# Optimization experiments

Hardware: AMD Instinct MI355X
Metric: run time of the kernel (lower is better)

The kernel has to match this reference:

```python
import jax, jax.numpy as jnp
import numpy as np

ALPHA = 0.2  # LeakyReLU negative slope
NEG_INF = -1e9


def setup_inputs() -> dict:
    key = jax.random.key(0)
    k1, k2, k3, k4 = jax.random.split(key, 4)
    B, N, IN, OUT = 8, 2048, 512, 32
    graph_input = jax.random.normal(k1, (B, N, IN), dtype=jnp.float32)
    adj = jax.random.randint(k2, (B, N, N), 0, 2, dtype=jnp.int32)
    W_fc = jax.random.normal(k3, (OUT, IN), dtype=jnp.float32) * (1.0 / np.sqrt(IN))
    W_attn = jax.random.normal(k4, (1, 2 * OUT), dtype=jnp.float32) * (1.0 / np.sqrt(2 * OUT))
    return {"graph_input": graph_input, "adj": adj, "W_fc": W_fc, "W_attn": W_attn}


def reference(graph_input, adj, W_fc, W_attn):
    # h: [B, N, 32]
    h = jnp.einsum('bni,oi->bno', graph_input, W_fc)
    out_dim = W_fc.shape[0]
    # attn_fc(cat(h_i, h_j)) is separable: a1.h_i + a2.h_j
    a1 = W_attn[0, :out_dim]   # [32]
    a2 = W_attn[0, out_dim:]   # [32]
    f1 = jnp.einsum('bno,o->bn', h, a1)  # [B, N]
    f2 = jnp.einsum('bno,o->bn', h, a2)  # [B, N]
    scores = jax.nn.leaky_relu(f1[:, :, None] + f2[:, None, :], negative_slope=ALPHA)  # [B,N,N]
    scores = jnp.where(adj == 0, NEG_INF, scores)
    attn = jax.nn.softmax(scores, axis=2)
    # NOTE: original multiplies attention with graph_input (not h)
    h_prime = jnp.einsum('bnm,bmi->bni', attn, graph_input)  # [B, N, IN]
    return jax.nn.elu(h_prime)  # concat=True path
```

## Files before the change

### kernel.cpp

```cpp
#include <hip/hip_runtime.h>
#include <hip/hip_bf16.h>

#define BATCH 8
#define NN    2048
#define FIN   512
#define FOUT  32
#define GALPHA 0.2f
#define NROW  128
#define NIT   32

typedef float  f32x4  __attribute__((ext_vector_type(4)));
typedef __bf16 bf16x8 __attribute__((ext_vector_type(8)));
typedef unsigned short u16;
typedef u16 u16x8 __attribute__((ext_vector_type(8)));

static __device__ __forceinline__ u16 f2bf(float f) {
    __hip_bfloat16 h = __float2bfloat16(f);
    union { __hip_bfloat16 h; u16 u; } c; c.h = h; return c.u;
}
static __device__ __forceinline__ float bf2f(u16 u) {
    union { u16 u; __hip_bfloat16 h; } c; c.u = u; return __bfloat162float(c.h);
}

__global__ void k_w12(const float* __restrict__ Wfc,
                      const float* __restrict__ Wat,
                      float* __restrict__ w1, float* __restrict__ w2) {
    int i = threadIdx.x;
    float s1 = 0.f, s2 = 0.f;
    #pragma unroll
    for (int o = 0; o < FOUT; o++) {
        float wv = Wfc[o * FIN + i];
        s1 += wv * Wat[o];
        s2 += wv * Wat[FOUT + o];
    }
    w1[i] = s1; w2[i] = s2;
}

__global__ void k_xtf(const float* __restrict__ x,
                      const float* __restrict__ w1, const float* __restrict__ w2,
                      __hip_bfloat16* __restrict__ xt,
                      float* __restrict__ f1, float* __restrict__ f2) {
    int bx = blockIdx.x;
    int it = bx & 7, mt = (bx >> 3) & 31, b = bx >> 8;
    int m0 = mt * 64, i0 = it * 64;
    __shared__ u16 tile[64][72];
    int tt = threadIdx.x;
    int mm = tt >> 3;
    int ic = (tt & 7) * 8;
    const float* xb = x + ((size_t)b * NN + m0) * FIN + i0;
    const f32x4* w1p = (const f32x4*)(w1 + i0 + ic);
    const f32x4* w2p = (const f32x4*)(w2 + i0 + ic);
    f32x4 wA = w1p[0], wB = w1p[1], wC = w2p[0], wD = w2p[1];
    float p1[2], p2[2];
    #pragma unroll
    for (int h = 0; h < 2; h++) {
        int m = mm + h * 32;
        const f32x4* src = (const f32x4*)(xb + (size_t)m * FIN + ic);
        f32x4 v0 = src[0], v1 = src[1];
        u16x8 pk;
        float s1 = 0.f, s2 = 0.f;
        #pragma unroll
        for (int j = 0; j < 4; j++) {
            pk[j] = f2bf(v0[j]); pk[4 + j] = f2bf(v1[j]);
            s1 += v0[j] * wA[j] + v1[j] * wB[j];
            s2 += v0[j] * wC[j] + v1[j] * wD[j];
        }
        p1[h] = s1; p2[h] = s2;
        *(u16x8*)&tile[m][ic] = pk;
    }
    #pragma unroll
    for (int off = 1; off < 8; off <<= 1) {
        p1[0] += __shfl_xor(p1[0], off); p1[1] += __shfl_xor(p1[1], off);
        p2[0] += __shfl_xor(p2[0], off); p2[1] += __shfl_xor(p2[1], off);
    }
    if ((tt & 7) == 0) {
        size_t r0 = (size_t)b * NN + m0 + mm;
        atomicAdd(&f1[r0], p1[0]);      atomicAdd(&f1[r0 + 32], p1[1]);
        atomicAdd(&f2[r0], p2[0]);      atomicAdd(&f2[r0 + 32], p2[1]);
    }
    __syncthreads();
    __hip_bfloat16* xtb = xt + ((size_t)b * FIN + i0) * NN + m0;
    int mc = (tt & 7) * 8;
    #pragma unroll
    for (int h = 0; h < 2; h++) {
        int ii = (tt >> 3) + h * 32;
        u16x8 v;
        #pragma unroll
        for (int j = 0; j < 8; j++) v[j] = tile[mc + j][ii];
        *(u16x8*)(xtb + (size_t)ii * NN + mc) = v;
    }
}

__global__ void k_pack(const int* __restrict__ adj, unsigned int* __restrict__ bits) {
    int row  = blockIdx.x * 4 + (threadIdx.x >> 6);
    int lane = threadIdx.x & 63;
    const int* p = adj + (size_t)row * NN + lane * 32;
    unsigned int bv = 0;
    #pragma unroll
    for (int j = 0; j < 8; j++) {
        int4 v = *(const int4*)(p + j * 4);
        bv |= (v.x != 0 ? 1u : 0u) << (j * 4 + 0);
        bv |= (v.y != 0 ? 1u : 0u) << (j * 4 + 1);
        bv |= (v.z != 0 ? 1u : 0u) << (j * 4 + 2);
        bv |= (v.w != 0 ? 1u : 0u) << (j * 4 + 3);
    }
    bits[(size_t)row * 64 + lane] = bv;
}

__global__ __launch_bounds__(512, 2) void k_main(
    const unsigned int* __restrict__ bits, const __hip_bfloat16* __restrict__ xt,
    const float* __restrict__ f1, const float* __restrict__ f2,
    float* __restrict__ out)
{
    const int bx = blockIdx.x;
    const int b = bx & 7, rt = (bx >> 3) & 15, it = bx >> 7;
    const int n0 = rt * NROW;
    const int i0 = it * 256;
    const int tid = threadIdx.x;
    const int lane = tid & 63, wv = tid >> 6;
    const int quad = lane >> 4, l15 = lane & 15;

    __shared__ u16 At[2][NROW * 64];
    __shared__ float rs[NROW];

    const int grow = tid >> 2;
    const int q4   = tid & 3;
    const unsigned short* bp = (const unsigned short*)bits
                               + ((size_t)(b * NN) + n0 + grow) * 128 + q4;
    const float* f2p = f2 + b * NN + q4 * 16;
    const float  f1v = f1[b * NN + n0 + grow];
    const int swz = grow & 7;
    u16* wp0 = &At[0][grow * 64 + (((q4 * 2) ^ swz) * 8)];
    u16* wp1 = &At[0][grow * 64 + (((q4 * 2 + 1) ^ swz) * 8)];
    float rpart = 0.f;

    const __hip_bfloat16* xtp = xt + ((size_t)(b * FIN) + i0 + wv * 32 + l15) * NN + quad * 8;

    f32x4 acc[8][2];
    #pragma unroll
    for (int s = 0; s < 8; s++) { acc[s][0] = (f32x4){0,0,0,0}; acc[s][1] = (f32x4){0,0,0,0}; }

    auto gen = [&](int buf, unsigned int bv, const f32x4* fr) {
        u16x8 pk0, pk1;
        #pragma unroll
        for (int e = 0; e < 16; e++) {
            float s  = f1v + fr[e >> 2][e & 3];
            float ls = fmaxf(s, GALPHA * s);
            float ev = ((bv >> e) & 1u) ? __expf(ls) : 0.f;
            u16 hb = f2bf(ev);
            rpart += bf2f(hb);
            if (e < 8) pk0[e] = hb; else pk1[e - 8] = hb;
        }
        *(u16x8*)(wp0 + buf * (NROW * 64)) = pk0;
        *(u16x8*)(wp1 + buf * (NROW * 64)) = pk1;
    };

    {
        unsigned int b0 = bp[0];
        f32x4 g0[4];
        #pragma unroll
        for (int j = 0; j < 4; j++) g0[j] = *(const f32x4*)(f2p + j * 4);
        gen(0, b0, g0);
    }
    unsigned int brng[2];
    f32x4 frng[2][4];
    brng[1] = bp[4];
    #pragma unroll
    for (int j = 0; j < 4; j++) frng[1][j] = *(const f32x4*)(f2p + 64 + j * 4);
    brng[0] = bp[8];
    #pragma unroll
    for (int j = 0; j < 4; j++) frng[0][j] = *(const f32x4*)(f2p + 128 + j * 4);

    bf16x8 Bc[2][2], Bn[2][2];
    #pragma unroll
    for (int ks = 0; ks < 2; ks++)
        #pragma unroll
        for (int c = 0; c < 2; c++)
            Bc[ks][c] = *(const bf16x8*)(xtp + ks * 32 + (size_t)(c * 16) * NN);
    __syncthreads();

    #pragma unroll 2
    for (int t = 0; t < NIT; t++) {
        const int cur = t & 1;
        if (t < NIT - 1) {
            const __hip_bfloat16* xk = xtp + (t + 1) * 64;
            #pragma unroll
            for (int ks = 0; ks < 2; ks++)
                #pragma unroll
                for (int c = 0; c < 2; c++)
                    Bn[ks][c] = *(const bf16x8*)(xk + ks * 32 + (size_t)(c * 16) * NN);
        }
        #pragma unroll
        for (int ks = 0; ks < 2; ks++) {
            #pragma unroll
            for (int s = 0; s < 8; s++) {
                const int row = s * 16 + l15;
                bf16x8 Af = *(const bf16x8*)&At[cur][row * 64 + (((ks * 4 + quad) ^ (row & 7)) * 8)];
                acc[s][0] = __builtin_amdgcn_mfma_f32_16x16x32_bf16(Af, Bc[ks][0], acc[s][0], 0, 0, 0);
                acc[s][1] = __builtin_amdgcn_mfma_f32_16x16x32_bf16(Af, Bc[ks][1], acc[s][1], 0, 0, 0);
            }
        }
        if (t < NIT - 1) {
            gen(1 - cur, brng[(t + 1) & 1], frng[(t + 1) & 1]);
            if (t < NIT - 2) {
                brng[t & 1] = bp[(t + 2) * 4];
                #pragma unroll
                for (int j = 0; j < 4; j++)
                    frng[t & 1][j] = *(const f32x4*)(f2p + (t + 2) * 64 + j * 4);
            }
        }
        asm volatile("s_waitcnt lgkmcnt(0)\ns_barrier" ::: "memory");
        #pragma unroll
        for (int ks = 0; ks < 2; ks++) {
            Bc[ks][0] = Bn[ks][0]; Bc[ks][1] = Bn[ks][1];
        }
    }

    rpart += __shfl_xor(rpart, 1);
    rpart += __shfl_xor(rpart, 2);
    if (q4 == 0) rs[grow] = 1.0f / rpart;
    __syncthreads();

    #pragma unroll
    for (int s = 0; s < 8; s++) {
        #pragma unroll
        for (int r = 0; r < 4; r++) {
            const int row = s * 16 + quad * 4 + r;
            const float inv = rs[row];
            float* op = out + ((size_t)b * NN + (n0 + row)) * FIN + i0 + wv * 32 + l15;
            #pragma unroll
            for (int c = 0; c < 2; c++) {
                float v = acc[s][c][r] * inv;
                v = v > 0.f ? v : (__expf(v) - 1.f);
                op[c * 16] = v;
            }
        }
    }
}

extern "C" void kernel_launch(void* const* d_in, const int* in_sizes, int n_in,
                              void* d_out, int out_size, void* d_ws, size_t ws_size,
                              hipStream_t stream) {
    const float* x   = (const float*)d_in[0];
    const int*   adj = (const int*)d_in[1];
    const float* Wfc = (const float*)d_in[2];
    const float* Wat = (const float*)d_in[3];
    float* out = (float*)d_out;

    float* w1 = (float*)d_ws;
    float* w2 = w1 + 512;
    float* f1 = w2 + 512;
    float* f2 = f1 + BATCH * NN;
    unsigned int* bits = (unsigned int*)(f2 + BATCH * NN);
    __hip_bfloat16* xt = (__hip_bfloat16*)(bits + (size_t)BATCH * NN * 64);

    hipMemsetAsync(f1, 0, (size_t)2 * BATCH * NN * sizeof(float), stream);
    hipLaunchKernelGGL(k_w12,  dim3(1),    dim3(512), 0, stream, Wfc, Wat, w1, w2);
    hipLaunchKernelGGL(k_xtf,  dim3(2048), dim3(256), 0, stream, x, w1, w2, xt, f1, f2);
    hipLaunchKernelGGL(k_pack, dim3(4096), dim3(256), 0, stream, adj, bits);
    hipLaunchKernelGGL(k_main, dim3(256),  dim3(512), 0, stream, bits, xt, f1, f2, out);
}
```

Measured before the change: 285.9 us.

## Halve row tile to 64 rows, doubling main-kernel grid to 512 blocks

```diff
diff --git a/kernel.cpp b/kernel.cpp
--- a/kernel.cpp
+++ b/kernel.cpp
@@ -6,12 +6,13 @@
 #define FIN   512
 #define FOUT  32
 #define GALPHA 0.2f
-#define NROW  128
+#define NROW  64
 #define NIT   32
 
 typedef float  f32x4  __attribute__((ext_vector_type(4)));
 typedef __bf16 bf16x8 __attribute__((ext_vector_type(8)));
 typedef unsigned short u16;
+typedef unsigned char  u8;
 typedef u16 u16x8 __attribute__((ext_vector_type(8)));
 
 static __device__ __forceinline__ u16 f2bf(float f) {
@@ -113,7 +114,7 @@
     float* __restrict__ out)
 {
     const int bx = blockIdx.x;
-    const int b = bx & 7, rt = (bx >> 3) & 15, it = bx >> 7;
+    const int b = bx & 7, rt = (bx >> 3) & 31, it = bx >> 8;
     const int n0 = rt * NROW;
     const int i0 = it * 256;
     const int tid = threadIdx.x;
@@ -123,53 +124,56 @@
     __shared__ u16 At[2][NROW * 64];
     __shared__ float rs[NROW];
 
-    const int grow = tid >> 2;
-    const int q4   = tid & 3;
-    const unsigned short* bp = (const unsigned short*)bits
-                               + ((size_t)(b * NN) + n0 + grow) * 128 + q4;
-    const float* f2p = f2 + b * NN + q4 * 16;
+    const int grow = tid >> 3;
+    const int oct  = tid & 7;
+    const u8*    bp  = (const u8*)bits + ((size_t)(b * NN) + n0 + grow) * 256 + oct;
+    const float* f2p = f2 + b * NN + oct * 8;
     const float  f1v = f1[b * NN + n0 + grow];
-    const int swz = grow & 7;
-    u16* wp0 = &At[0][grow * 64 + (((q4 * 2) ^ swz) * 8)];
-    u16* wp1 = &At[0][grow * 64 + (((q4 * 2 + 1) ^ swz) * 8)];
+    u16* wp = &At[0][grow * 64 + ((oct ^ (grow & 7)) * 8)];
     float rpart = 0.f;
 
     const __hip_bfloat16* xtp = xt + ((size_t)(b * FIN) + i0 + wv * 32 + l15) * NN + quad * 8;
 
-    f32x4 acc[8][2];
-    #pragma unroll
-    for (int s = 0; s < 8; s++) { acc[s][0] = (f32x4){0,0,0,0}; acc[s][1] = (f32x4){0,0,0,0}; }
-
-    auto gen = [&](int buf, unsigned int bv, const f32x4* fr) {
-        u16x8 pk0, pk1;
-        #pragma unroll
-        for (int e = 0; e < 16; e++) {
-            float s  = f1v + fr[e >> 2][e & 3];
+    f32x4 acc[4][2];
+    #pragma unroll
+    for (int s = 0; s < 4; s++) { acc[s][0] = (f32x4){0,0,0,0}; acc[s][1] = (f32x4){0,0,0,0}; }
+
+    auto gen = [&](int buf, unsigned int bv, f32x4 fa, f32x4 fb) {
+        u16x8 pk;
+        #pragma unroll
+        for (int e = 0; e < 8; e++) {
+            float s  = f1v + ((e < 4) ? fa[e & 3] : fb[e & 3]);
             float ls = fmaxf(s, GALPHA * s);
             float ev = ((bv >> e) & 1u) ? __expf(ls) : 0.f;
             u16 hb = f2bf(ev);
             rpart += bf2f(hb);
-            if (e < 8) pk0[e] = hb; else pk1[e - 8] = hb;
-        }
-        *(u16x8*)(wp0 + buf * (NROW * 64)) = pk0;
-        *(u16x8*)(wp1 + buf * (NROW * 64)) = pk1;
+            pk[e] = hb;
+        }
+        *(u16x8*)(wp + buf * (NROW * 64)) = pk;
+    };
+
+    auto mfma_step = [&](int buf, const bf16x8 B[2][2]) {
+        #pragma unroll
+        for (int ks = 0; ks < 2; ks++) {
+            #pragma unroll
+            for (int s = 0; s < 4; s++) {
+                const int row = s * 16 + l15;
+                bf16x8 Af = *(const bf16x8*)&At[buf][row * 64 + (((ks * 4 + quad) ^ (row & 7)) * 8)];
+                acc[s][0] = __builtin_amdgcn_mfma_f32_16x16x32_bf16(Af, B[ks][0], acc[s][0], 0, 0, 0);
+                acc[s][1] = __builtin_amdgcn_mfma_f32_16x16x32_bf16(Af, B[ks][1], acc[s][1], 0, 0, 0);
+            }
+        }
     };
 
     {
         unsigned int b0 = bp[0];
-        f32x4 g0[4];
-        #pragma unroll
-        for (int j = 0; j < 4; j++) g0[j] = *(const f32x4*)(f2p + j * 4);
-        gen(0, b0, g0);
-    }
-    unsigned int brng[2];
-    f32x4 frng[2][4];
-    brng[1] = bp[4];
-    #pragma unroll
-    for (int j = 0; j < 4; j++) frng[1][j] = *(const f32x4*)(f2p + 64 + j * 4);
-    brng[0] = bp[8];
-    #pragma unroll
-    for (int j = 0; j < 4; j++) frng[0][j] = *(const f32x4*)(f2p + 128 + j * 4);
+        f32x4 ga = *(const f32x4*)(f2p);
+        f32x4 gb = *(const f32x4*)(f2p + 4);
+        gen(0, b0, ga, gb);
+    }
+    unsigned int bA = bp[8],  bB = bp[16];
+    f32x4 fA0 = *(const f32x4*)(f2p + 64),  fA1 = *(const f32x4*)(f2p + 68);
+    f32x4 fB0 = *(const f32x4*)(f2p + 128), fB1 = *(const f32x4*)(f2p + 132);
 
     bf16x8 Bc[2][2], Bn[2][2];
     #pragma unroll
@@ -179,50 +183,53 @@
             Bc[ks][c] = *(const bf16x8*)(xtp + ks * 32 + (size_t)(c * 16) * NN);
     __syncthreads();
 
-    #pragma unroll 2
-    for (int t = 0; t < NIT; t++) {
-        const int cur = t & 1;
-        if (t < NIT - 1) {
-            const __hip_bfloat16* xk = xtp + (t + 1) * 64;
+    for (int t = 0; t < NIT; t += 2) {
+        {
+            const __hip_bfloat16* xk = xtp + (size_t)(t + 1) * 64;
             #pragma unroll
-            for (int ks = 0; ks < 2; ks++)
+            for (int ks = 0; ks < 2; ks++) {
+                Bn[ks][0] = *(const bf16x8*)(xk + ks * 32);
+                Bn[ks][1] = *(const bf16x8*)(xk + ks * 32 + (size_t)16 * NN);
+            }
+            mfma_step(0, Bc);
+            gen(1, bA, fA0, fA1);
+            if (t + 3 < NIT) {
+                bA  = bp[(t + 3) * 8];
+                fA0 = *(const f32x4*)(f2p + (t + 3) * 64);
+                fA1 = *(const f32x4*)(f2p + (t + 3) * 64 + 4);
+            }
+            asm volatile("s_waitcnt lgkmcnt(0)\ns_barrier" ::: "memory");
+        }
+        {
+            if (t + 2 < NIT) {
+                const __hip_bfloat16* xk = xtp + (size_t)(t + 2) * 64;
                 #pragma unroll
-                for (int c = 0; c < 2; c++)
-                    Bn[ks][c] = *(const bf16x8*)(xk + ks * 32 + (size_t)(c * 16) * NN);
-        }
-        #pragma unroll
-        for (int ks = 0; ks < 2; ks++) {
-            #pragma unroll
-            for (int s = 0; s < 8; s++) {
-                const int row = s * 16 + l15;
-                bf16x8 Af = *(const bf16x8*)&At[cur][row * 64 + (((ks * 4 + quad) ^ (row & 7)) * 8)];
-                acc[s][0] = __builtin_amdgcn_mfma_f32_16x16x32_bf16(Af, Bc[ks][0], acc[s][0], 0, 0, 0);
-                acc[s][1] = __builtin_amdgcn_mfma_f32_16x16x32_bf16(Af, Bc[ks][1], acc[s][1], 0, 0, 0);
-            }
-        }
-        if (t < NIT - 1) {
-            gen(1 - cur, brng[(t + 1) & 1], frng[(t + 1) & 1]);
-            if (t < NIT - 2) {
-                brng[t & 1] = bp[(t + 2) * 4];
-                #pragma unroll
-                for (int j = 0; j < 4; j++)
-                    frng[t & 1][j] = *(const f32x4*)(f2p + (t + 2) * 64 + j * 4);
-            }
-        }
-        asm volatile("s_waitcnt lgkmcnt(0)\ns_barrier" ::: "memory");
-        #pragma unroll
-        for (int ks = 0; ks < 2; ks++) {
-            Bc[ks][0] = Bn[ks][0]; Bc[ks][1] = Bn[ks][1];
+                for (int ks = 0; ks < 2; ks++) {
+                    Bc[ks][0] = *(const bf16x8*)(xk + ks * 32);
+                    Bc[ks][1] = *(const bf16x8*)(xk + ks * 32 + (size_t)16 * NN);
+                }
+            }
+            mfma_step(1, Bn);
+            if (t + 2 < NIT) {
+                gen(0, bB, fB0, fB1);
+                if (t + 4 < NIT) {
+                    bB  = bp[(t + 4) * 8];
+                    fB0 = *(const f32x4*)(f2p + (t + 4) * 64);
+                    fB1 = *(const f32x4*)(f2p + (t + 4) * 64 + 4);
+                }
+                asm volatile("s_waitcnt lgkmcnt(0)\ns_barrier" ::: "memory");
+            }
         }
     }
 
     rpart += __shfl_xor(rpart, 1);
     rpart += __shfl_xor(rpart, 2);
-    if (q4 == 0) rs[grow] = 1.0f / rpart;
+    rpart += __shfl_xor(rpart, 4);
+    if (oct == 0) rs[grow] = 1.0f / rpart;
     __syncthreads();
 
     #pragma unroll
-    for (int s = 0; s < 8; s++) {
+    for (int s = 0; s < 4; s++) {
         #pragma unroll
         for (int r = 0; r < 4; r++) {
             const int row = s * 16 + quad * 4 + r;
@@ -258,5 +265,5 @@
     hipLaunchKernelGGL(k_w12,  dim3(1),    dim3(512), 0, stream, Wfc, Wat, w1, w2);
     hipLaunchKernelGGL(k_xtf,  dim3(2048), dim3(256), 0, stream, x, w1, w2, xt, f1, f2);
     hipLaunchKernelGGL(k_pack, dim3(4096), dim3(256), 0, stream, adj, bits);
-    hipLaunchKernelGGL(k_main, dim3(256),  dim3(512), 0, stream, bits, xt, f1, f2, out);
-}
+    hipLaunchKernelGGL(k_main, dim3(512),  dim3(512), 0, stream, bits, xt, f1, f2, out);
+}
```

Result: slower. 319.4 us (+11.7%).

## Warp-specialize main kernel into producer/consumer waves with LDS ring buffer

Applied to the files above, without the earlier changes.

```diff
diff --git a/kernel.cpp b/kernel.cpp
--- a/kernel.cpp
+++ b/kernel.cpp
@@ -6,8 +6,9 @@
 #define FIN   512
 #define FOUT  32
 #define GALPHA 0.2f
-#define NROW  128
+#define NROW  64
 #define NIT   32
+#define NSLOT 4
 
 typedef float  f32x4  __attribute__((ext_vector_type(4)));
 typedef __bf16 bf16x8 __attribute__((ext_vector_type(8)));
@@ -33,7 +34,8 @@
         s1 += wv * Wat[o];
         s2 += wv * Wat[FOUT + o];
     }
-    w1[i] = s1; w2[i] = s2;
+    const float LOG2E = 1.4426950408889634f;
+    w1[i] = s1 * LOG2E; w2[i] = s2 * LOG2E;
 }
 
 __global__ void k_xtf(const float* __restrict__ x,
@@ -107,132 +109,132 @@
     bits[(size_t)row * 64 + lane] = bv;
 }
 
-__global__ __launch_bounds__(512, 2) void k_main(
+__global__ __launch_bounds__(512, 4) void k_main(
     const unsigned int* __restrict__ bits, const __hip_bfloat16* __restrict__ xt,
     const float* __restrict__ f1, const float* __restrict__ f2,
     float* __restrict__ out)
 {
     const int bx = blockIdx.x;
-    const int b = bx & 7, rt = (bx >> 3) & 15, it = bx >> 7;
+    const int b = bx & 7, rt = (bx >> 3) & 31, it = bx >> 8;
     const int n0 = rt * NROW;
     const int i0 = it * 256;
     const int tid = threadIdx.x;
-    const int lane = tid & 63, wv = tid >> 6;
-    const int quad = lane >> 4, l15 = lane & 15;
-
-    __shared__ u16 At[2][NROW * 64];
+    const int wv = tid >> 6;
+    const int lane = tid & 63, quad = lane >> 4, l15 = lane & 15;
+
+    __shared__ u16 At[NSLOT][NROW * 64];
     __shared__ float rs[NROW];
-
-    const int grow = tid >> 2;
-    const int q4   = tid & 3;
-    const unsigned short* bp = (const unsigned short*)bits
-                               + ((size_t)(b * NN) + n0 + grow) * 128 + q4;
-    const float* f2p = f2 + b * NN + q4 * 16;
-    const float  f1v = f1[b * NN + n0 + grow];
-    const int swz = grow & 7;
-    u16* wp0 = &At[0][grow * 64 + (((q4 * 2) ^ swz) * 8)];
-    u16* wp1 = &At[0][grow * 64 + (((q4 * 2 + 1) ^ swz) * 8)];
-    float rpart = 0.f;
-
-    const __hip_bfloat16* xtp = xt + ((size_t)(b * FIN) + i0 + wv * 32 + l15) * NN + quad * 8;
-
-    f32x4 acc[8][2];
-    #pragma unroll
-    for (int s = 0; s < 8; s++) { acc[s][0] = (f32x4){0,0,0,0}; acc[s][1] = (f32x4){0,0,0,0}; }
-
-    auto gen = [&](int buf, unsigned int bv, const f32x4* fr) {
-        u16x8 pk0, pk1;
-        #pragma unroll
-        for (int e = 0; e < 16; e++) {
-            float s  = f1v + fr[e >> 2][e & 3];
-            float ls = fmaxf(s, GALPHA * s);
-            float ev = ((bv >> e) & 1u) ? __expf(ls) : 0.f;
-            u16 hb = f2bf(ev);
-            rpart += bf2f(hb);
-            if (e < 8) pk0[e] = hb; else pk1[e - 8] = hb;
-        }
-        *(u16x8*)(wp0 + buf * (NROW * 64)) = pk0;
-        *(u16x8*)(wp1 + buf * (NROW * 64)) = pk1;
-    };
-
-    {
-        unsigned int b0 = bp[0];
-        f32x4 g0[4];
-        #pragma unroll
-        for (int j = 0; j < 4; j++) g0[j] = *(const f32x4*)(f2p + j * 4);
-        gen(0, b0, g0);
-    }
-    unsigned int brng[2];
-    f32x4 frng[2][4];
-    brng[1] = bp[4];
-    #pragma unroll
-    for (int j = 0; j < 4; j++) frng[1][j] = *(const f32x4*)(f2p + 64 + j * 4);
-    brng[0] = bp[8];
-    #pragma unroll
-    for (int j = 0; j < 4; j++) frng[0][j] = *(const f32x4*)(f2p + 128 + j * 4);
-
-    bf16x8 Bc[2][2], Bn[2][2];
-    #pragma unroll
-    for (int ks = 0; ks < 2; ks++)
-        #pragma unroll
-        for (int c = 0; c < 2; c++)
-            Bc[ks][c] = *(const bf16x8*)(xtp + ks * 32 + (size_t)(c * 16) * NN);
+    __shared__ int prod_done[NSLOT], cons_done[NSLOT];
+
+    if (tid < NSLOT) { prod_done[tid] = 0; cons_done[tid] = 0; }
     __syncthreads();
 
-    #pragma unroll 2
-    for (int t = 0; t < NIT; t++) {
-        const int cur = t & 1;
-        if (t < NIT - 1) {
-            const __hip_bfloat16* xk = xtp + (t + 1) * 64;
+    f32x4 acc[4][4];
+    #pragma unroll
+    for (int s = 0; s < 4; s++)
+        #pragma unroll
+        for (int c = 0; c < 4; c++) acc[s][c] = (f32x4){0.f, 0.f, 0.f, 0.f};
+
+    if (wv < 4) {
+        const int row = tid >> 2;
+        const int o2  = tid & 3;
+        const u16*   bp  = (const u16*)bits + ((size_t)(b * NN) + n0 + row) * 128 + o2;
+        const float* f2p = f2 + b * NN + o2 * 16;
+        const float  f1v = f1[b * NN + n0 + row];
+        const int swz = row & 7;
+        u16* wpa = &At[0][row * 64 + (((o2 * 2)     ^ swz) * 8)];
+        u16* wpb = &At[0][row * 64 + (((o2 * 2 + 1) ^ swz) * 8)];
+        float rpart = 0.f;
+
+        unsigned int bvN = bp[0];
+        f32x4 fN0 = *(const f32x4*)(f2p),     fN1 = *(const f32x4*)(f2p + 4);
+        f32x4 fN2 = *(const f32x4*)(f2p + 8), fN3 = *(const f32x4*)(f2p + 12);
+
+        for (int t = 0; t < NIT; t++) {
+            const int s = t & (NSLOT - 1);
+            unsigned int bv = bvN;
+            f32x4 fc[4] = {fN0, fN1, fN2, fN3};
+            if (t < NIT - 1) {
+                bvN = bp[(t + 1) * 4];
+                const float* fp = f2p + (t + 1) * 64;
+                fN0 = *(const f32x4*)(fp);     fN1 = *(const f32x4*)(fp + 4);
+                fN2 = *(const f32x4*)(fp + 8); fN3 = *(const f32x4*)(fp + 12);
+            }
+            if (t >= NSLOT) {
+                const int tgt = 4 * (t >> 2);
+                while (__hip_atomic_load(&cons_done[s], __ATOMIC_ACQUIRE,
+                                         __HIP_MEMORY_SCOPE_WORKGROUP) < tgt) {}
+            }
+            u16x8 pk0, pk1;
+            #pragma unroll
+            for (int e = 0; e < 16; e++) {
+                float sc = f1v + fc[e >> 2][e & 3];
+                float ls = fmaxf(sc, GALPHA * sc);
+                float ev = ((bv >> e) & 1u) ? __builtin_amdgcn_exp2f(ls) : 0.f;
+                u16 hb = f2bf(ev);
+                rpart += bf2f(hb);
+                if (e < 8) pk0[e] = hb; else pk1[e - 8] = hb;
+            }
+            *(u16x8*)(wpa + s * (NROW * 64)) = pk0;
+            *(u16x8*)(wpb + s * (NROW * 64)) = pk1;
+            if (lane == 0) {}
+            if ((tid & 63) == 0) {}
+            if (lane == 0)
+                __hip_atomic_fetch_add(&prod_done[s], 1, __ATOMIC_RELEASE,
+                                       __HIP_MEMORY_SCOPE_WORKGROUP);
+        }
+        rpart += __shfl_xor(rpart, 1);
+        rpart += __shfl_xor(rpart, 2);
+        if (o2 == 0) rs[row] = 1.0f / rpart;
+    } else {
+        const int cw = wv - 4;
+        const __hip_bfloat16* xtp = xt + ((size_t)(b * FIN) + i0 + cw * 64 + l15) * NN + quad * 8;
+        for (int t = 0; t < NIT; t++) {
+            const int s = t & (NSLOT - 1);
+            const int tgt = 4 * ((t >> 2) + 1);
+            while (__hip_atomic_load(&prod_done[s], __ATOMIC_ACQUIRE,
+                                     __HIP_MEMORY_SCOPE_WORKGROUP) < tgt) {}
+            const __hip_bfloat16* xk = xtp + (size_t)t * 64;
+            bf16x8 B[2][4];
             #pragma unroll
             for (int ks = 0; ks < 2; ks++)
                 #pragma unroll
-                for (int c = 0; c < 2; c++)
-                    Bn[ks][c] = *(const bf16x8*)(xk + ks * 32 + (size_t)(c * 16) * NN);
-        }
-        #pragma unroll
-        for (int ks = 0; ks < 2; ks++) {
-            #pragma unroll
-            for (int s = 0; s < 8; s++) {
-                const int row = s * 16 + l15;
-                bf16x8 Af = *(const bf16x8*)&At[cur][row * 64 + (((ks * 4 + quad) ^ (row & 7)) * 8)];
-                acc[s][0] = __builtin_amdgcn_mfma_f32_16x16x32_bf16(Af, Bc[ks][0], acc[s][0], 0, 0, 0);
-                acc[s][1] = __builtin_amdgcn_mfma_f32_16x16x32_bf16(Af, Bc[ks][1], acc[s][1], 0, 0, 0);
-            }
-        }
-        if (t < NIT - 1) {
-            gen(1 - cur, brng[(t + 1) & 1], frng[(t + 1) & 1]);
-            if (t < NIT - 2) {
-                brng[t & 1] = bp[(t + 2) * 4];
+                for (int c = 0; c < 4; c++)
+                    B[ks][c] = *(const bf16x8*)(xk + ks * 32 + (size_t)(c * 16) * NN);
+            #pragma unroll
+            for (int ks = 0; ks < 2; ks++) {
                 #pragma unroll
-                for (int j = 0; j < 4; j++)
-                    frng[t & 1][j] = *(const f32x4*)(f2p + (t + 2) * 64 + j * 4);
-            }
-        }
-        asm volatile("s_waitcnt lgkmcnt(0)\ns_barrier" ::: "memory");
-        #pragma unroll
-        for (int ks = 0; ks < 2; ks++) {
-            Bc[ks][0] = Bn[ks][0]; Bc[ks][1] = Bn[ks][1];
-        }
-    }
-
-    rpart += __shfl_xor(rpart, 1);
-    rpart += __shfl_xor(rpart, 2);
-    if (q4 == 0) rs[grow] = 1.0f / rpart;
+                for (int st = 0; st < 4; st++) {
+                    const int row = st * 16 + l15;
+                    bf16x8 Af = *(const bf16x8*)&At[s][row * 64 + (((ks * 4 + quad) ^ (row & 7)) * 8)];
+                    #pragma unroll
+                    for (int c = 0; c < 4; c++)
+                        acc[st][c] = __builtin_amdgcn_mfma_f32_16x16x32_bf16(Af, B[ks][c], acc[st][c], 0, 0, 0);
+                }
+            }
+            if (lane == 0)
+                __hip_atomic_fetch_add(&cons_done[s], 1, __ATOMIC_RELEASE,
+                                       __HIP_MEMORY_SCOPE_WORKGROUP);
+        }
+    }
+
     __syncthreads();
 
-    #pragma unroll
-    for (int s = 0; s < 8; s++) {
-        #pragma unroll
-        for (int r = 0; r < 4; r++) {
-            const int row = s * 16 + quad * 4 + r;
-            const float inv = rs[row];
-            float* op = out + ((size_t)b * NN + (n0 + row)) * FIN + i0 + wv * 32 + l15;
-            #pragma unroll
-            for (int c = 0; c < 2; c++) {
-                float v = acc[s][c][r] * inv;
-                v = v > 0.f ? v : (__expf(v) - 1.f);
-                op[c * 16] = v;
+    if (wv >= 4) {
+        const int cw = wv - 4;
+        #pragma unroll
+        for (int st = 0; st < 4; st++) {
+            #pragma unroll
+            for (int r = 0; r < 4; r++) {
+                const int row = st * 16 + quad * 4 + r;
+                const float inv = rs[row];
+                float* op = out + ((size_t)b * NN + (n0 + row)) * FIN + i0 + cw * 64 + l15;
+                #pragma unroll
+                for (int c = 0; c < 4; c++) {
+                    float v = acc[st][c][r] * inv;
+                    v = v > 0.f ? v : (__expf(v) - 1.f);
+                    op[c * 16] = v;
+                }
             }
         }
     }
@@ -258,5 +260,5 @@
     hipLaunchKernelGGL(k_w12,  dim3(1),    dim3(512), 0, stream, Wfc, Wat, w1, w2);
     hipLaunchKernelGGL(k_xtf,  dim3(2048), dim3(256), 0, stream, x, w1, w2, xt, f1, f2);
     hipLaunchKernelGGL(k_pack, dim3(4096), dim3(256), 0, stream, adj, bits);
-    hipLaunchKernelGGL(k_main, dim3(256),  dim3(512), 0, stream, bits, xt, f1, f2, out);
-}
+    hipLaunchKernelGGL(k_main, dim3(512),  dim3(512), 0, stream, bits, xt, f1, f2, out);
+}
```

Result: slower. 309.5 us (+8.2%).
